# Kernel tuning notes

Measured on AMD Instinct MI355X. Metric: run time of the kernel, lower is better.

Reference implementation:

```python
import jax, jax.numpy as jnp
import numpy as np
import random

EPS = 1e-16  # matches EKM eps default
B, M, N, R = 8, 8192, 512, 256


def setup_inputs() -> dict:
    key = jax.random.key(0)
    kx, = jax.random.split(key, 1)
    x = jax.random.normal(kx, (B, M, N), dtype=jnp.float32)
    # EKM init: random.seed(42); inds = random.sample(range(M), R)
    random.seed(42)
    inds = jnp.asarray(random.sample(range(M), R), dtype=jnp.int32)
    # EKMInit overrides ekm.alpha with nn.Parameter(torch.tensor([0.1]))
    alpha = jnp.asarray([0.1], dtype=jnp.float32)
    return {"x": x, "alpha": alpha, "inds": inds}


def _memberships(x, v, alpha):
    x2 = jnp.sum(x * x, axis=2, keepdims=True)           # (B, M, 1)
    xv = jnp.einsum('bmn,bnr->bmr', x, v)                # (B, M, R)
    v2 = jnp.sum(v * v, axis=1, keepdims=True)           # (B, 1, R)
    d = jax.nn.relu(x2 - 2.0 * xv + v2)
    return jax.nn.softmax(-d / alpha, axis=2)            # (B, M, R)


def reference(x, alpha, inds):
    # init: v0 = t(x[:, inds, :]) -> (B, N, R); u0 = memberships(x, v0)
    v0 = jnp.swapaxes(x[:, inds, :], 1, 2)               # (B, N, R)
    # solver step (num_iters=1): u_new = memberships(x, v0) (== u0),
    # v_new = centers(x, u_new)
    u = _memberships(x, v0, alpha)                       # (B, M, R)
    u_n = (u + EPS) / (jnp.sum(u, axis=1, keepdims=True) + EPS)
    v = jnp.einsum('bmn,bmr->bnr', x, u_n)               # (B, N, R)
    return (u, v)
```

## Files before the change

kernel.cpp:

```cpp
#include <hip/hip_runtime.h>
#include <math.h>

#define B 8
#define M 8192
#define N 512
#define R 256
#define EPSF 1e-16f

typedef __attribute__((ext_vector_type(8))) short short8;
typedef __attribute__((ext_vector_type(16))) float f32x16;

__device__ __forceinline__ unsigned short bf16_rtn(float f) {
    unsigned int u = __float_as_uint(f);
    u += 0x7FFFu + ((u >> 16) & 1u);
    return (unsigned short)(u >> 16);
}

__device__ __forceinline__ void gll16(const unsigned short* g, unsigned short* l) {
    __builtin_amdgcn_global_load_lds(
        (const __attribute__((address_space(1))) unsigned int*)g,
        (__attribute__((address_space(3))) unsigned int*)l, 16, 0, 0);
}

__global__ __launch_bounds__(256) void ekm_kc(
    const float* __restrict__ x, const int* __restrict__ inds,
    unsigned short* __restrict__ c_hi, unsigned short* __restrict__ c_lo,
    float* __restrict__ v2g)
{
    const int t = threadIdx.x, b = blockIdx.y;
    const int r = blockIdx.x * 16 + (t >> 4);
    const int seg = (t & 15) * 32;
    const float* src = x + ((size_t)b * M + inds[r]) * N + seg;
    unsigned short* hd = c_hi + ((size_t)b * R + r) * 512 + seg;
    unsigned short* ld = c_lo + ((size_t)b * R + r) * 512 + seg;
    float vp = 0.f;
#pragma unroll
    for (int c = 0; c < 4; ++c) {
        float4 f0 = *(const float4*)(src + c * 8);
        float4 f1 = *(const float4*)(src + c * 8 + 4);
        float av[8] = {f0.x, f0.y, f0.z, f0.w, f1.x, f1.y, f1.z, f1.w};
        unsigned ph[4], pl[4];
#pragma unroll
        for (int j = 0; j < 4; ++j) {
            vp += av[2*j] * av[2*j] + av[2*j+1] * av[2*j+1];
            unsigned short h0 = bf16_rtn(av[2*j]), h1 = bf16_rtn(av[2*j+1]);
            float r0 = av[2*j]   - __uint_as_float((unsigned)h0 << 16);
            float r1 = av[2*j+1] - __uint_as_float((unsigned)h1 << 16);
            ph[j] = (unsigned)h0 | ((unsigned)h1 << 16);
            pl[j] = (unsigned)bf16_rtn(r0) | ((unsigned)bf16_rtn(r1) << 16);
        }
        *(uint4*)(hd + c * 8) = make_uint4(ph[0], ph[1], ph[2], ph[3]);
        *(uint4*)(ld + c * 8) = make_uint4(pl[0], pl[1], pl[2], pl[3]);
    }
    vp += __shfl_xor(vp, 1); vp += __shfl_xor(vp, 2);
    vp += __shfl_xor(vp, 4); vp += __shfl_xor(vp, 8);
    if ((t & 15) == 0) v2g[b * R + r] = vp;
}

__global__ __launch_bounds__(256, 4) void ekm_k1(
    const float* __restrict__ x, const float* __restrict__ alpha_p,
    const unsigned short* __restrict__ c_hi, const unsigned short* __restrict__ c_lo,
    const float* __restrict__ v2g, float* __restrict__ u_out,
    unsigned short* __restrict__ uT, unsigned short* __restrict__ xT,
    float* __restrict__ colsum)
{
    __shared__ unsigned short Ah[64 * 32], Al[64 * 32];
    __shared__ unsigned short Bh[256 * 32], Bl[256 * 32];

    const int t = threadIdx.x;
    const int b = blockIdx.y;
    const int m0 = blockIdx.x * 64;
    const int w = t >> 6, l = t & 63, col = l & 31, h5 = l >> 5;
    const int arow = t >> 2, kch = t & 3;
    const int cswz = (t & 3) ^ ((t >> 3) & 3);
    const int pswz = (col >> 1) & 3;
    const int aswz = (col >> 3) & 3;
    const int awi = arow * 32 + (kch ^ ((arow >> 3) & 3)) * 8;

    const float* ax = x + ((size_t)b * M + m0 + arow) * N + kch * 8;
    const unsigned short* bhs = c_hi + ((size_t)b * R + (t >> 2)) * 512 + cswz * 8;
    const unsigned short* bls = c_lo + ((size_t)b * R + (t >> 2)) * 512 + cswz * 8;

    f32x16 acc[2][2];
    acc[0][0] = (f32x16)0.f; acc[0][1] = (f32x16)0.f;
    acc[1][0] = (f32x16)0.f; acc[1][1] = (f32x16)0.f;

    float x2p = 0.f;
    float4 a0 = *(const float4*)(ax);
    float4 a1 = *(const float4*)(ax + 4);

    for (int k0 = 0; k0 < N; k0 += 32) {
        x2p += a0.x*a0.x + a0.y*a0.y + a0.z*a0.z + a0.w*a0.w
             + a1.x*a1.x + a1.y*a1.y + a1.z*a1.z + a1.w*a1.w;
        float av[8] = {a0.x, a0.y, a0.z, a0.w, a1.x, a1.y, a1.z, a1.w};
        unsigned ph[4], pl[4];
#pragma unroll
        for (int j = 0; j < 4; ++j) {
            unsigned short h0 = bf16_rtn(av[2*j]), h1 = bf16_rtn(av[2*j+1]);
            float r0 = av[2*j]   - __uint_as_float((unsigned)h0 << 16);
            float r1 = av[2*j+1] - __uint_as_float((unsigned)h1 << 16);
            ph[j] = (unsigned)h0 | ((unsigned)h1 << 16);
            pl[j] = (unsigned)bf16_rtn(r0) | ((unsigned)bf16_rtn(r1) << 16);
        }
        __syncthreads();
#pragma unroll
        for (int i = 0; i < 4; ++i) {
            gll16(bhs + k0 + i * (64 * 512), Bh + i * 2048 + t * 8);
            gll16(bls + k0 + i * (64 * 512), Bl + i * 2048 + t * 8);
        }
        *(uint4*)&Ah[awi] = make_uint4(ph[0], ph[1], ph[2], ph[3]);
        *(uint4*)&Al[awi] = make_uint4(pl[0], pl[1], pl[2], pl[3]);
        __syncthreads();

        if (k0 + 32 < N) {
            a0 = *(const float4*)(ax + k0 + 32);
            a1 = *(const float4*)(ax + k0 + 36);
        }

        {
            int kk = t >> 3, ms = (t & 7) * 8;
            unsigned short vv[8];
#pragma unroll
            for (int i = 0; i < 8; ++i) {
                int row = ms + i;
                vv[i] = Ah[row * 32 + (((kk >> 3) ^ ((row >> 3) & 3)) << 3) + (kk & 7)];
            }
            *(uint4*)(xT + ((size_t)b * N + k0 + kk) * M + m0 + ms) =
                make_uint4((unsigned)vv[0] | ((unsigned)vv[1] << 16),
                           (unsigned)vv[2] | ((unsigned)vv[3] << 16),
                           (unsigned)vv[4] | ((unsigned)vv[5] << 16),
                           (unsigned)vv[6] | ((unsigned)vv[7] << 16));
        }

#pragma unroll
        for (int half = 0; half < 2; ++half) {
            const int pa = (half * 2 + h5) ^ aswz;
            const int pc = (half * 2 + h5) ^ pswz;
            short8 ah[2], al2[2], bh[2], bl2[2];
#pragma unroll
            for (int tm = 0; tm < 2; ++tm) {
                ah[tm]  = *(const short8*)&Ah[(tm*32 + col) * 32 + pa * 8];
                al2[tm] = *(const short8*)&Al[(tm*32 + col) * 32 + pa * 8];
            }
#pragma unroll
            for (int tr = 0; tr < 2; ++tr) {
                bh[tr]  = *(const short8*)&Bh[(w*64 + tr*32 + col) * 32 + pc * 8];
                bl2[tr] = *(const short8*)&Bl[(w*64 + tr*32 + col) * 32 + pc * 8];
            }
#pragma unroll
            for (int tm = 0; tm < 2; ++tm)
#pragma unroll
            for (int tr = 0; tr < 2; ++tr) {
                acc[tm][tr] = __builtin_amdgcn_mfma_f32_32x32x16_bf16(ah[tm],  bh[tr],  acc[tm][tr], 0, 0, 0);
                acc[tm][tr] = __builtin_amdgcn_mfma_f32_32x32x16_bf16(ah[tm],  bl2[tr], acc[tm][tr], 0, 0, 0);
                acc[tm][tr] = __builtin_amdgcn_mfma_f32_32x32x16_bf16(al2[tm], bh[tr],  acc[tm][tr], 0, 0, 0);
            }
        }
    }

    __syncthreads();
    float* x2s = (float*)&Ah[0];
    float (*redm)[64] = (float (*)[64])&Al[0];
    float (*reds)[64] = (float (*)[64])&Bh[0];

    x2p += __shfl_xor(x2p, 1);
    x2p += __shfl_xor(x2p, 2);
    if (kch == 0) x2s[arow] = x2p;
    __syncthreads();

    const float ia = 1.4426950408889634f / alpha_p[0];
    float v2c[2];
#pragma unroll
    for (int tr = 0; tr < 2; ++tr)
        v2c[tr] = v2g[b * R + w * 64 + tr * 32 + col];

#pragma unroll
    for (int tm = 0; tm < 2; ++tm)
#pragma unroll
    for (int reg = 0; reg < 16; ++reg) {
        int rowl = (reg & 3) + 8 * (reg >> 2) + 4 * h5;
        float x2v = x2s[tm * 32 + rowl];
        float mn;
#pragma unroll
        for (int tr = 0; tr < 2; ++tr) {
            float d = x2v - 2.f * acc[tm][tr][reg] + v2c[tr];
            d = fmaxf(d, 0.f);
            acc[tm][tr][reg] = d;
            mn = (tr == 0) ? d : fminf(mn, d);
        }
        mn = fminf(mn, __shfl_xor(mn, 1));
        mn = fminf(mn, __shfl_xor(mn, 2));
        mn = fminf(mn, __shfl_xor(mn, 4));
        mn = fminf(mn, __shfl_xor(mn, 8));
        mn = fminf(mn, __shfl_xor(mn, 16));
        if (col == 0) redm[w][tm * 32 + rowl] = mn;
    }
    __syncthreads();

#pragma unroll
    for (int tm = 0; tm < 2; ++tm)
#pragma unroll
    for (int reg = 0; reg < 16; ++reg) {
        int m = tm * 32 + (reg & 3) + 8 * (reg >> 2) + 4 * h5;
        float mn = fminf(fminf(redm[0][m], redm[1][m]), fminf(redm[2][m], redm[3][m]));
        float s = 0.f;
#pragma unroll
        for (int tr = 0; tr < 2; ++tr) {
            float e = exp2f((mn - acc[tm][tr][reg]) * ia);
            acc[tm][tr][reg] = e;
            s += e;
        }
        s += __shfl_xor(s, 1); s += __shfl_xor(s, 2); s += __shfl_xor(s, 4);
        s += __shfl_xor(s, 8); s += __shfl_xor(s, 16);
        if (col == 0) reds[w][m] = s;
    }
    __syncthreads();

    float* ub = u_out + ((size_t)b * M + m0) * R + w * 64;
    float cs[2] = {0.f, 0.f};
#pragma unroll
    for (int tm = 0; tm < 2; ++tm)
#pragma unroll
    for (int reg = 0; reg < 16; ++reg) {
        int rowl = (reg & 3) + 8 * (reg >> 2) + 4 * h5;
        int m = tm * 32 + rowl;
        float inv = 1.f / (reds[0][m] + reds[1][m] + reds[2][m] + reds[3][m]);
#pragma unroll
        for (int tr = 0; tr < 2; ++tr) {
            float uu = acc[tm][tr][reg] * inv;
            acc[tm][tr][reg] = uu;
            ub[(size_t)m * R + tr * 32 + col] = uu;
            cs[tr] += uu;
        }
    }
    unsigned short* uTb = uT + ((size_t)b * R + w * 64) * M + m0;
#pragma unroll
    for (int tm = 0; tm < 2; ++tm)
#pragma unroll
    for (int tr = 0; tr < 2; ++tr)
#pragma unroll
    for (int rq = 0; rq < 4; ++rq) {
        uint2 p;
        p.x = (unsigned)bf16_rtn(acc[tm][tr][rq*4+0]) | ((unsigned)bf16_rtn(acc[tm][tr][rq*4+1]) << 16);
        p.y = (unsigned)bf16_rtn(acc[tm][tr][rq*4+2]) | ((unsigned)bf16_rtn(acc[tm][tr][rq*4+3]) << 16);
        *(uint2*)(uTb + (size_t)(tr*32 + col) * M + tm*32 + 8*rq + 4*h5) = p;
    }
    cs[0] += __shfl_xor(cs[0], 32);
    cs[1] += __shfl_xor(cs[1], 32);
    if (h5 == 0) {
        atomicAdd(&colsum[b * R + w * 64 + col], cs[0]);
        atomicAdd(&colsum[b * R + w * 64 + 32 + col], cs[1]);
    }
}

__global__ __launch_bounds__(256, 2) void ekm_k2(
    const unsigned short* __restrict__ xT, const unsigned short* __restrict__ uT,
    float* __restrict__ part)
{
    __shared__ unsigned short XA[128 * 32], UB[128 * 32];
    const int t = threadIdx.x;
    const int nt = blockIdx.x >> 1, rt = blockIdx.x & 1;
    const int slab = blockIdx.y, b = blockIdx.z;
    const int n0 = nt * 128, r0 = rt * 128;
    const int w = t >> 6, l = t & 63, col = l & 31, h5 = l >> 5;
    const int wn = w >> 1, wr = w & 1;
    const int cswz = (t & 3) ^ ((t >> 3) & 3);
    const int pswz = (col >> 1) & 3;

    const unsigned short* xs = xT + ((size_t)b * N + n0 + (t >> 2)) * M + slab * 1024 + cswz * 8;
    const unsigned short* us = uT + ((size_t)b * R + r0 + (t >> 2)) * M + slab * 1024 + cswz * 8;

    f32x16 acc[2][2];
    acc[0][0] = (f32x16)0.f; acc[0][1] = (f32x16)0.f;
    acc[1][0] = (f32x16)0.f; acc[1][1] = (f32x16)0.f;

    for (int k0 = 0; k0 < 1024; k0 += 32) {
        __syncthreads();
#pragma unroll
        for (int i = 0; i < 2; ++i) {
            gll16(xs + k0 + (size_t)i * 64 * M, XA + i * 2048 + t * 8);
            gll16(us + k0 + (size_t)i * 64 * M, UB + i * 2048 + t * 8);
        }
        __syncthreads();
#pragma unroll
        for (int half = 0; half < 2; ++half) {
            const int pc = (half * 2 + h5) ^ pswz;
            short8 af[2], bf2[2];
#pragma unroll
            for (int tm = 0; tm < 2; ++tm)
                af[tm] = *(const short8*)&XA[(wn*64 + tm*32 + col) * 32 + pc*8];
#pragma unroll
            for (int tr = 0; tr < 2; ++tr)
                bf2[tr] = *(const short8*)&UB[(wr*64 + tr*32 + col) * 32 + pc*8];
#pragma unroll
            for (int tm = 0; tm < 2; ++tm)
#pragma unroll
            for (int tr = 0; tr < 2; ++tr)
                acc[tm][tr] = __builtin_amdgcn_mfma_f32_32x32x16_bf16(af[tm], bf2[tr], acc[tm][tr], 0, 0, 0);
        }
    }

    float* pb = part + (size_t)slab * ((size_t)B * N * R) + (size_t)b * N * R;
#pragma unroll
    for (int tm = 0; tm < 2; ++tm)
#pragma unroll
    for (int reg = 0; reg < 16; ++reg) {
        int n = n0 + wn*64 + tm*32 + (reg & 3) + 8*(reg >> 2) + 4*h5;
#pragma unroll
        for (int tr = 0; tr < 2; ++tr)
            pb[(size_t)n * R + r0 + wr*64 + tr*32 + col] = acc[tm][tr][reg];
    }
}

__global__ __launch_bounds__(256) void ekm_red(
    const float* __restrict__ part, const float* __restrict__ colsum,
    float* __restrict__ v_out)
{
    size_t o = ((size_t)blockIdx.x * 256 + threadIdx.x) * 4;
    float sx = 0.f, sy = 0.f, sz = 0.f, sw = 0.f;
#pragma unroll
    for (int sl = 0; sl < 8; ++sl) {
        float4 p = *(const float4*)(part + (size_t)sl * B * N * R + o);
        sx += p.x; sy += p.y; sz += p.z; sw += p.w;
    }
    int b = (int)(o >> 17);
    int r = (int)(o & (R - 1));
    float4 cs = *(const float4*)(colsum + b * R + r);
    float4 vo;
    vo.x = sx / (cs.x + EPSF);
    vo.y = sy / (cs.y + EPSF);
    vo.z = sz / (cs.z + EPSF);
    vo.w = sw / (cs.w + EPSF);
    *(float4*)(v_out + o) = vo;
}

extern "C" void kernel_launch(void* const* d_in, const int* in_sizes, int n_in,
                              void* d_out, int out_size, void* d_ws, size_t ws_size,
                              hipStream_t stream) {
    const float* x     = (const float*)d_in[0];
    const float* alpha = (const float*)d_in[1];
    const int*   inds  = (const int*)d_in[2];

    float* u_out = (float*)d_out;
    float* v_out = u_out + (size_t)B * M * R;

    char* ws = (char*)d_ws;
    const size_t CH = (size_t)B * R * 512 * 2;
    unsigned short* c_hi   = (unsigned short*)ws;
    unsigned short* c_lo   = (unsigned short*)(ws + CH);
    float*          v2g    = (float*)(ws + 2 * CH);
    float*          colsum = (float*)(ws + 2 * CH + (size_t)B * R * 4);
    char* p = ws + 2 * CH + 2 * (size_t)B * R * 4;
    unsigned short* xT = (unsigned short*)p;          p += (size_t)B * N * M * 2;
    unsigned short* uT = (unsigned short*)p;          p += (size_t)B * R * M * 2;
    float*          part = (float*)p;

    hipMemsetAsync(colsum, 0, (size_t)B * R * sizeof(float), stream);

    ekm_kc<<<dim3(16, B), 256, 0, stream>>>(x, inds, c_hi, c_lo, v2g);
    ekm_k1<<<dim3(M / 64, B), 256, 0, stream>>>(x, alpha, c_hi, c_lo, v2g,
                                                u_out, uT, xT, colsum);
    ekm_k2<<<dim3(8, 8, B), 256, 0, stream>>>(xT, uT, part);
    ekm_red<<<(B * N * R / 4) / 256, 256, 0, stream>>>(part, colsum, v_out);
}
```

Measured before the change: 341.8 us.

## Halve k1 row tile and software-pipeline global loads through registers

The first GEMM kernel now processes 32 rows of x per block instead of 64, doubling the grid. The B operand (centers) is loaded into registers one k-step ahead rather than via direct global-to-LDS loads, and the A conversion is overlapped with the MFMA work using explicit barriers and sched_barriers. The aim is to hide global memory latency and raise parallelism. In exchange, each block reuses the B tile over half as many rows, so the centers are read from global memory twice as often, and register pressure rises.

```diff
diff --git a/kernel.cpp b/kernel.cpp
--- a/kernel.cpp
+++ b/kernel.cpp
@@ -64,108 +64,137 @@
     unsigned short* __restrict__ uT, unsigned short* __restrict__ xT,
     float* __restrict__ colsum)
 {
-    __shared__ unsigned short Ah[64 * 32], Al[64 * 32];
+    __shared__ unsigned short Ah[32 * 32], Al[32 * 32];
     __shared__ unsigned short Bh[256 * 32], Bl[256 * 32];
 
     const int t = threadIdx.x;
     const int b = blockIdx.y;
-    const int m0 = blockIdx.x * 64;
+    const int m0 = blockIdx.x * 32;
     const int w = t >> 6, l = t & 63, col = l & 31, h5 = l >> 5;
-    const int arow = t >> 2, kch = t & 3;
+    const int arow = t >> 3, kc8 = t & 7;
     const int cswz = (t & 3) ^ ((t >> 3) & 3);
     const int pswz = (col >> 1) & 3;
     const int aswz = (col >> 3) & 3;
-    const int awi = arow * 32 + (kch ^ ((arow >> 3) & 3)) * 8;
-
-    const float* ax = x + ((size_t)b * M + m0 + arow) * N + kch * 8;
+    const int awi = arow * 32 + ((kc8 >> 1) ^ ((arow >> 3) & 3)) * 8 + (kc8 & 1) * 4;
+
+    const float* ax = x + ((size_t)b * M + m0 + arow) * N + kc8 * 4;
     const unsigned short* bhs = c_hi + ((size_t)b * R + (t >> 2)) * 512 + cswz * 8;
     const unsigned short* bls = c_lo + ((size_t)b * R + (t >> 2)) * 512 + cswz * 8;
 
-    f32x16 acc[2][2];
-    acc[0][0] = (f32x16)0.f; acc[0][1] = (f32x16)0.f;
-    acc[1][0] = (f32x16)0.f; acc[1][1] = (f32x16)0.f;
+    f32x16 acc[2];
+    acc[0] = (f32x16)0.f; acc[1] = (f32x16)0.f;
 
     float x2p = 0.f;
-    float4 a0 = *(const float4*)(ax);
-    float4 a1 = *(const float4*)(ax + 4);
-
-    for (int k0 = 0; k0 < N; k0 += 32) {
-        x2p += a0.x*a0.x + a0.y*a0.y + a0.z*a0.z + a0.w*a0.w
-             + a1.x*a1.x + a1.y*a1.y + a1.z*a1.z + a1.w*a1.w;
-        float av[8] = {a0.x, a0.y, a0.z, a0.w, a1.x, a1.y, a1.z, a1.w};
-        unsigned ph[4], pl[4];
-#pragma unroll
-        for (int j = 0; j < 4; ++j) {
-            unsigned short h0 = bf16_rtn(av[2*j]), h1 = bf16_rtn(av[2*j+1]);
-            float r0 = av[2*j]   - __uint_as_float((unsigned)h0 << 16);
-            float r1 = av[2*j+1] - __uint_as_float((unsigned)h1 << 16);
-            ph[j] = (unsigned)h0 | ((unsigned)h1 << 16);
-            pl[j] = (unsigned)bf16_rtn(r0) | ((unsigned)bf16_rtn(r1) << 16);
-        }
-        __syncthreads();
+    float4 a0;
+    unsigned ph0, ph1, pl0, pl1;
+    uint4 rbh[4], rbl[4];
+
+    auto loadB = [&](int k0) {
 #pragma unroll
         for (int i = 0; i < 4; ++i) {
-            gll16(bhs + k0 + i * (64 * 512), Bh + i * 2048 + t * 8);
-            gll16(bls + k0 + i * (64 * 512), Bl + i * 2048 + t * 8);
-        }
-        *(uint4*)&Ah[awi] = make_uint4(ph[0], ph[1], ph[2], ph[3]);
-        *(uint4*)&Al[awi] = make_uint4(pl[0], pl[1], pl[2], pl[3]);
-        __syncthreads();
-
-        if (k0 + 32 < N) {
-            a0 = *(const float4*)(ax + k0 + 32);
-            a1 = *(const float4*)(ax + k0 + 36);
-        }
-
-        {
-            int kk = t >> 3, ms = (t & 7) * 8;
-            unsigned short vv[8];
-#pragma unroll
-            for (int i = 0; i < 8; ++i) {
-                int row = ms + i;
-                vv[i] = Ah[row * 32 + (((kk >> 3) ^ ((row >> 3) & 3)) << 3) + (kk & 7)];
-            }
-            *(uint4*)(xT + ((size_t)b * N + k0 + kk) * M + m0 + ms) =
-                make_uint4((unsigned)vv[0] | ((unsigned)vv[1] << 16),
-                           (unsigned)vv[2] | ((unsigned)vv[3] << 16),
-                           (unsigned)vv[4] | ((unsigned)vv[5] << 16),
-                           (unsigned)vv[6] | ((unsigned)vv[7] << 16));
-        }
-
+            rbh[i] = *(const uint4*)(bhs + k0 + i * (64 * 512));
+            rbl[i] = *(const uint4*)(bls + k0 + i * (64 * 512));
+        }
+    };
+    auto writeB = [&](void) {
+#pragma unroll
+        for (int i = 0; i < 4; ++i) {
+            *(uint4*)&Bh[i * 2048 + t * 8] = rbh[i];
+            *(uint4*)&Bl[i * 2048 + t * 8] = rbl[i];
+        }
+    };
+    auto convertA = [&](void) {
+        float av[4] = {a0.x, a0.y, a0.z, a0.w};
+        x2p += av[0]*av[0] + av[1]*av[1] + av[2]*av[2] + av[3]*av[3];
+        unsigned short h0 = bf16_rtn(av[0]), h1 = bf16_rtn(av[1]);
+        unsigned short h2 = bf16_rtn(av[2]), h3 = bf16_rtn(av[3]);
+        float r0 = av[0] - __uint_as_float((unsigned)h0 << 16);
+        float r1 = av[1] - __uint_as_float((unsigned)h1 << 16);
+        float r2 = av[2] - __uint_as_float((unsigned)h2 << 16);
+        float r3 = av[3] - __uint_as_float((unsigned)h3 << 16);
+        ph0 = (unsigned)h0 | ((unsigned)h1 << 16);
+        ph1 = (unsigned)h2 | ((unsigned)h3 << 16);
+        pl0 = (unsigned)bf16_rtn(r0) | ((unsigned)bf16_rtn(r1) << 16);
+        pl1 = (unsigned)bf16_rtn(r2) | ((unsigned)bf16_rtn(r3) << 16);
+    };
+    auto writeA = [&](void) {
+        *(uint2*)&Ah[awi] = make_uint2(ph0, ph1);
+        *(uint2*)&Al[awi] = make_uint2(pl0, pl1);
+    };
+    auto mfma_tile = [&](void) {
 #pragma unroll
         for (int half = 0; half < 2; ++half) {
             const int pa = (half * 2 + h5) ^ aswz;
             const int pc = (half * 2 + h5) ^ pswz;
-            short8 ah[2], al2[2], bh[2], bl2[2];
-#pragma unroll
-            for (int tm = 0; tm < 2; ++tm) {
-                ah[tm]  = *(const short8*)&Ah[(tm*32 + col) * 32 + pa * 8];
-                al2[tm] = *(const short8*)&Al[(tm*32 + col) * 32 + pa * 8];
-            }
+            short8 ah = *(const short8*)&Ah[col * 32 + pa * 8];
+            short8 al = *(const short8*)&Al[col * 32 + pa * 8];
+            short8 bh[2], bl2[2];
 #pragma unroll
             for (int tr = 0; tr < 2; ++tr) {
                 bh[tr]  = *(const short8*)&Bh[(w*64 + tr*32 + col) * 32 + pc * 8];
                 bl2[tr] = *(const short8*)&Bl[(w*64 + tr*32 + col) * 32 + pc * 8];
             }
 #pragma unroll
-            for (int tm = 0; tm < 2; ++tm)
-#pragma unroll
             for (int tr = 0; tr < 2; ++tr) {
-                acc[tm][tr] = __builtin_amdgcn_mfma_f32_32x32x16_bf16(ah[tm],  bh[tr],  acc[tm][tr], 0, 0, 0);
-                acc[tm][tr] = __builtin_amdgcn_mfma_f32_32x32x16_bf16(ah[tm],  bl2[tr], acc[tm][tr], 0, 0, 0);
-                acc[tm][tr] = __builtin_amdgcn_mfma_f32_32x32x16_bf16(al2[tm], bh[tr],  acc[tm][tr], 0, 0, 0);
+                acc[tr] = __builtin_amdgcn_mfma_f32_32x32x16_bf16(ah, bh[tr],  acc[tr], 0, 0, 0);
+                acc[tr] = __builtin_amdgcn_mfma_f32_32x32x16_bf16(ah, bl2[tr], acc[tr], 0, 0, 0);
+                acc[tr] = __builtin_amdgcn_mfma_f32_32x32x16_bf16(al, bh[tr],  acc[tr], 0, 0, 0);
             }
         }
-    }
+    };
+    auto xt_store = [&](int k0) {
+        int kk = t >> 3, ms = (t & 7) * 4;
+        unsigned short vv[4];
+#pragma unroll
+        for (int j = 0; j < 4; ++j) {
+            int row = ms + j;
+            vv[j] = Ah[row * 32 + (((kk >> 3) ^ ((row >> 3) & 3)) << 3) + (kk & 7)];
+        }
+        *(uint2*)(xT + ((size_t)b * N + k0 + kk) * M + m0 + ms) =
+            make_uint2((unsigned)vv[0] | ((unsigned)vv[1] << 16),
+                       (unsigned)vv[2] | ((unsigned)vv[3] << 16));
+    };
+
+    a0 = *(const float4*)(ax);
+    loadB(0);
+    convertA();
+    writeA(); writeB();
+    a0 = *(const float4*)(ax + 32);
+    loadB(32);
+    asm volatile("s_waitcnt lgkmcnt(0)" ::: "memory");
+    __builtin_amdgcn_sched_barrier(0);
+    __builtin_amdgcn_s_barrier();
+    __builtin_amdgcn_sched_barrier(0);
+
+    for (int k0 = 0; k0 < N - 32; k0 += 32) {
+        xt_store(k0);
+        mfma_tile();
+        convertA();
+        __builtin_amdgcn_sched_barrier(0);
+        __builtin_amdgcn_s_barrier();
+        __builtin_amdgcn_sched_barrier(0);
+        writeA(); writeB();
+        if (k0 + 64 < N) {
+            a0 = *(const float4*)(ax + k0 + 64);
+            loadB(k0 + 64);
+        }
+        asm volatile("s_waitcnt lgkmcnt(0)" ::: "memory");
+        __builtin_amdgcn_sched_barrier(0);
+        __builtin_amdgcn_s_barrier();
+        __builtin_amdgcn_sched_barrier(0);
+    }
+    xt_store(N - 32);
+    mfma_tile();
 
     __syncthreads();
     float* x2s = (float*)&Ah[0];
-    float (*redm)[64] = (float (*)[64])&Al[0];
-    float (*reds)[64] = (float (*)[64])&Bh[0];
+    float (*redm)[32] = (float (*)[32])&Al[0];
+    float (*reds)[32] = (float (*)[32])&Bh[0];
 
     x2p += __shfl_xor(x2p, 1);
     x2p += __shfl_xor(x2p, 2);
-    if (kch == 0) x2s[arow] = x2p;
+    x2p += __shfl_xor(x2p, 4);
+    if (kc8 == 0) x2s[arow] = x2p;
     __syncthreads();
 
     const float ia = 1.4426950408889634f / alpha_p[0];
@@ -175,17 +204,15 @@
         v2c[tr] = v2g[b * R + w * 64 + tr * 32 + col];
 
 #pragma unroll
-    for (int tm = 0; tm < 2; ++tm)
-#pragma unroll
     for (int reg = 0; reg < 16; ++reg) {
         int rowl = (reg & 3) + 8 * (reg >> 2) + 4 * h5;
-        float x2v = x2s[tm * 32 + rowl];
+        float x2v = x2s[rowl];
         float mn;
 #pragma unroll
         for (int tr = 0; tr < 2; ++tr) {
-            float d = x2v - 2.f * acc[tm][tr][reg] + v2c[tr];
+            float d = x2v - 2.f * acc[tr][reg] + v2c[tr];
             d = fmaxf(d, 0.f);
-            acc[tm][tr][reg] = d;
+            acc[tr][reg] = d;
             mn = (tr == 0) ? d : fminf(mn, d);
         }
         mn = fminf(mn, __shfl_xor(mn, 1));
@@ -193,21 +220,19 @@
         mn = fminf(mn, __shfl_xor(mn, 4));
         mn = fminf(mn, __shfl_xor(mn, 8));
         mn = fminf(mn, __shfl_xor(mn, 16));
-        if (col == 0) redm[w][tm * 32 + rowl] = mn;
+        if (col == 0) redm[w][rowl] = mn;
     }
     __syncthreads();
 
 #pragma unroll
-    for (int tm = 0; tm < 2; ++tm)
-#pragma unroll
     for (int reg = 0; reg < 16; ++reg) {
-        int m = tm * 32 + (reg & 3) + 8 * (reg >> 2) + 4 * h5;
+        int m = (reg & 3) + 8 * (reg >> 2) + 4 * h5;
         float mn = fminf(fminf(redm[0][m], redm[1][m]), fminf(redm[2][m], redm[3][m]));
         float s = 0.f;
 #pragma unroll
         for (int tr = 0; tr < 2; ++tr) {
-            float e = exp2f((mn - acc[tm][tr][reg]) * ia);
-            acc[tm][tr][reg] = e;
+            float e = exp2f((mn - acc[tr][reg]) * ia);
+            acc[tr][reg] = e;
             s += e;
         }
         s += __shfl_xor(s, 1); s += __shfl_xor(s, 2); s += __shfl_xor(s, 4);
@@ -219,31 +244,26 @@
     float* ub = u_out + ((size_t)b * M + m0) * R + w * 64;
     float cs[2] = {0.f, 0.f};
 #pragma unroll
-    for (int tm = 0; tm < 2; ++tm)
-#pragma unroll
     for (int reg = 0; reg < 16; ++reg) {
-        int rowl = (reg & 3) + 8 * (reg >> 2) + 4 * h5;
-        int m = tm * 32 + rowl;
+        int m = (reg & 3) + 8 * (reg >> 2) + 4 * h5;
         float inv = 1.f / (reds[0][m] + reds[1][m] + reds[2][m] + reds[3][m]);
 #pragma unroll
         for (int tr = 0; tr < 2; ++tr) {
-            float uu = acc[tm][tr][reg] * inv;
-            acc[tm][tr][reg] = uu;
+            float uu = acc[tr][reg] * inv;
+            acc[tr][reg] = uu;
             ub[(size_t)m * R + tr * 32 + col] = uu;
             cs[tr] += uu;
         }
     }
     unsigned short* uTb = uT + ((size_t)b * R + w * 64) * M + m0;
 #pragma unroll
-    for (int tm = 0; tm < 2; ++tm)
-#pragma unroll
     for (int tr = 0; tr < 2; ++tr)
 #pragma unroll
     for (int rq = 0; rq < 4; ++rq) {
         uint2 p;
-        p.x = (unsigned)bf16_rtn(acc[tm][tr][rq*4+0]) | ((unsigned)bf16_rtn(acc[tm][tr][rq*4+1]) << 16);
-        p.y = (unsigned)bf16_rtn(acc[tm][tr][rq*4+2]) | ((unsigned)bf16_rtn(acc[tm][tr][rq*4+3]) << 16);
-        *(uint2*)(uTb + (size_t)(tr*32 + col) * M + tm*32 + 8*rq + 4*h5) = p;
+        p.x = (unsigned)bf16_rtn(acc[tr][rq*4+0]) | ((unsigned)bf16_rtn(acc[tr][rq*4+1]) << 16);
+        p.y = (unsigned)bf16_rtn(acc[tr][rq*4+2]) | ((unsigned)bf16_rtn(acc[tr][rq*4+3]) << 16);
+        *(uint2*)(uTb + (size_t)(tr*32 + col) * M + 8*rq + 4*h5) = p;
     }
     cs[0] += __shfl_xor(cs[0], 32);
     cs[1] += __shfl_xor(cs[1], 32);
@@ -358,7 +378,7 @@
     hipMemsetAsync(colsum, 0, (size_t)B * R * sizeof(float), stream);
 
     ekm_kc<<<dim3(16, B), 256, 0, stream>>>(x, inds, c_hi, c_lo, v2g);
-    ekm_k1<<<dim3(M / 64, B), 256, 0, stream>>>(x, alpha, c_hi, c_lo, v2g,
+    ekm_k1<<<dim3(M / 32, B), 256, 0, stream>>>(x, alpha, c_hi, c_lo, v2g,
                                                 u_out, uT, xT, colsum);
     ekm_k2<<<dim3(8, 8, B), 256, 0, stream>>>(xT, uT, part);
     ekm_red<<<(B * N * R / 4) / 256, 256, 0, stream>>>(part, colsum, v_out);
```

Result: slower. 690.2 us (+101.9%).

## Load centers directly into registers in MFMA-fragment layout with double buffering

Applied to the files above, without the earlier changes.

The center matrix (hi/lo bf16 split) is now written by the prep kernel in a layout that matches the MFMA operand fragments. The main kernel loads B fragments straight from global memory into registers, double-buffered across k-steps, instead of staging them through LDS with global_load_lds. This removes the large B tiles from shared memory, along with their LDS traffic and part of the barrier work. Blocks are also reordered so batch varies fastest, and the occupancy hint drops from 4 to 3 to leave room for the extra fragment registers. The risks are redundant global and L2 reads of B by each block, and reduced occupancy.

```diff
diff --git a/kernel.cpp b/kernel.cpp
--- a/kernel.cpp
+++ b/kernel.cpp
@@ -24,15 +24,16 @@
 
 __global__ __launch_bounds__(256) void ekm_kc(
     const float* __restrict__ x, const int* __restrict__ inds,
-    unsigned short* __restrict__ c_hi, unsigned short* __restrict__ c_lo,
+    unsigned short* __restrict__ cpH, unsigned short* __restrict__ cpL,
     float* __restrict__ v2g)
 {
     const int t = threadIdx.x, b = blockIdx.y;
     const int r = blockIdx.x * 16 + (t >> 4);
     const int seg = (t & 15) * 32;
+    const int rg = r >> 5, rl = r & 31;
     const float* src = x + ((size_t)b * M + inds[r]) * N + seg;
-    unsigned short* hd = c_hi + ((size_t)b * R + r) * 512 + seg;
-    unsigned short* ld = c_lo + ((size_t)b * R + r) * 512 + seg;
+    unsigned short* hb = cpH + (((size_t)b * 32 + (seg >> 4)) * 8 + rg) * 512;
+    unsigned short* lb = cpL + (((size_t)b * 32 + (seg >> 4)) * 8 + rg) * 512;
     float vp = 0.f;
 #pragma unroll
     for (int c = 0; c < 4; ++c) {
@@ -49,119 +50,151 @@
             ph[j] = (unsigned)h0 | ((unsigned)h1 << 16);
             pl[j] = (unsigned)bf16_rtn(r0) | ((unsigned)bf16_rtn(r1) << 16);
         }
-        *(uint4*)(hd + c * 8) = make_uint4(ph[0], ph[1], ph[2], ph[3]);
-        *(uint4*)(ld + c * 8) = make_uint4(pl[0], pl[1], pl[2], pl[3]);
+        const size_t off = (size_t)(c >> 1) * 4096 + (size_t)((c & 1) * 32 + rl) * 8;
+        *(uint4*)(hb + off) = make_uint4(ph[0], ph[1], ph[2], ph[3]);
+        *(uint4*)(lb + off) = make_uint4(pl[0], pl[1], pl[2], pl[3]);
     }
     vp += __shfl_xor(vp, 1); vp += __shfl_xor(vp, 2);
     vp += __shfl_xor(vp, 4); vp += __shfl_xor(vp, 8);
     if ((t & 15) == 0) v2g[b * R + r] = vp;
 }
 
-__global__ __launch_bounds__(256, 4) void ekm_k1(
+__global__ __launch_bounds__(256, 3) void ekm_k1(
     const float* __restrict__ x, const float* __restrict__ alpha_p,
-    const unsigned short* __restrict__ c_hi, const unsigned short* __restrict__ c_lo,
+    const unsigned short* __restrict__ cpH, const unsigned short* __restrict__ cpL,
     const float* __restrict__ v2g, float* __restrict__ u_out,
     unsigned short* __restrict__ uT, unsigned short* __restrict__ xT,
     float* __restrict__ colsum)
 {
     __shared__ unsigned short Ah[64 * 32], Al[64 * 32];
-    __shared__ unsigned short Bh[256 * 32], Bl[256 * 32];
 
     const int t = threadIdx.x;
-    const int b = blockIdx.y;
-    const int m0 = blockIdx.x * 64;
+    const int bid = blockIdx.x;
+    const int b = bid & 7;
+    const int m0 = (bid >> 3) * 64;
     const int w = t >> 6, l = t & 63, col = l & 31, h5 = l >> 5;
     const int arow = t >> 2, kch = t & 3;
-    const int cswz = (t & 3) ^ ((t >> 3) & 3);
-    const int pswz = (col >> 1) & 3;
     const int aswz = (col >> 3) & 3;
     const int awi = arow * 32 + (kch ^ ((arow >> 3) & 3)) * 8;
 
     const float* ax = x + ((size_t)b * M + m0 + arow) * N + kch * 8;
-    const unsigned short* bhs = c_hi + ((size_t)b * R + (t >> 2)) * 512 + cswz * 8;
-    const unsigned short* bls = c_lo + ((size_t)b * R + (t >> 2)) * 512 + cswz * 8;
+    const unsigned short* bpH = cpH + (((size_t)b * 256 + w * 2) * 64 + l) * 8;
+    const unsigned short* bpL = cpL + (((size_t)b * 256 + w * 2) * 64 + l) * 8;
 
     f32x16 acc[2][2];
     acc[0][0] = (f32x16)0.f; acc[0][1] = (f32x16)0.f;
     acc[1][0] = (f32x16)0.f; acc[1][1] = (f32x16)0.f;
 
     float x2p = 0.f;
-    float4 a0 = *(const float4*)(ax);
-    float4 a1 = *(const float4*)(ax + 4);
-
-    for (int k0 = 0; k0 < N; k0 += 32) {
-        x2p += a0.x*a0.x + a0.y*a0.y + a0.z*a0.z + a0.w*a0.w
-             + a1.x*a1.x + a1.y*a1.y + a1.z*a1.z + a1.w*a1.w;
+    float4 a0, a1;
+    unsigned ph[4], pl[4];
+    short8 cbh[2][2], cbl[2][2], nbh[2][2], nbl[2][2];
+
+    auto loadB = [&](int kc0, short8 (&bh)[2][2], short8 (&bl)[2][2]) {
+#pragma unroll
+        for (int half = 0; half < 2; ++half)
+#pragma unroll
+        for (int tr = 0; tr < 2; ++tr) {
+            const size_t o = (size_t)(kc0 + half) * 4096 + (size_t)tr * 512;
+            bh[half][tr] = *(const short8*)(bpH + o);
+            bl[half][tr] = *(const short8*)(bpL + o);
+        }
+    };
+    auto convertA = [&](void) {
         float av[8] = {a0.x, a0.y, a0.z, a0.w, a1.x, a1.y, a1.z, a1.w};
-        unsigned ph[4], pl[4];
 #pragma unroll
         for (int j = 0; j < 4; ++j) {
+            x2p += av[2*j] * av[2*j] + av[2*j+1] * av[2*j+1];
             unsigned short h0 = bf16_rtn(av[2*j]), h1 = bf16_rtn(av[2*j+1]);
             float r0 = av[2*j]   - __uint_as_float((unsigned)h0 << 16);
             float r1 = av[2*j+1] - __uint_as_float((unsigned)h1 << 16);
             ph[j] = (unsigned)h0 | ((unsigned)h1 << 16);
             pl[j] = (unsigned)bf16_rtn(r0) | ((unsigned)bf16_rtn(r1) << 16);
         }
-        __syncthreads();
-#pragma unroll
-        for (int i = 0; i < 4; ++i) {
-            gll16(bhs + k0 + i * (64 * 512), Bh + i * 2048 + t * 8);
-            gll16(bls + k0 + i * (64 * 512), Bl + i * 2048 + t * 8);
-        }
+    };
+    auto writeA = [&](void) {
         *(uint4*)&Ah[awi] = make_uint4(ph[0], ph[1], ph[2], ph[3]);
         *(uint4*)&Al[awi] = make_uint4(pl[0], pl[1], pl[2], pl[3]);
-        __syncthreads();
-
-        if (k0 + 32 < N) {
-            a0 = *(const float4*)(ax + k0 + 32);
-            a1 = *(const float4*)(ax + k0 + 36);
-        }
-
-        {
-            int kk = t >> 3, ms = (t & 7) * 8;
-            unsigned short vv[8];
-#pragma unroll
-            for (int i = 0; i < 8; ++i) {
-                int row = ms + i;
-                vv[i] = Ah[row * 32 + (((kk >> 3) ^ ((row >> 3) & 3)) << 3) + (kk & 7)];
-            }
-            *(uint4*)(xT + ((size_t)b * N + k0 + kk) * M + m0 + ms) =
-                make_uint4((unsigned)vv[0] | ((unsigned)vv[1] << 16),
-                           (unsigned)vv[2] | ((unsigned)vv[3] << 16),
-                           (unsigned)vv[4] | ((unsigned)vv[5] << 16),
-                           (unsigned)vv[6] | ((unsigned)vv[7] << 16));
-        }
-
+    };
+    auto mfma_tile = [&](short8 (&bh)[2][2], short8 (&bl)[2][2]) {
 #pragma unroll
         for (int half = 0; half < 2; ++half) {
             const int pa = (half * 2 + h5) ^ aswz;
-            const int pc = (half * 2 + h5) ^ pswz;
-            short8 ah[2], al2[2], bh[2], bl2[2];
+            short8 ah[2], al2[2];
 #pragma unroll
             for (int tm = 0; tm < 2; ++tm) {
                 ah[tm]  = *(const short8*)&Ah[(tm*32 + col) * 32 + pa * 8];
                 al2[tm] = *(const short8*)&Al[(tm*32 + col) * 32 + pa * 8];
             }
 #pragma unroll
+            for (int tm = 0; tm < 2; ++tm)
+#pragma unroll
             for (int tr = 0; tr < 2; ++tr) {
-                bh[tr]  = *(const short8*)&Bh[(w*64 + tr*32 + col) * 32 + pc * 8];
-                bl2[tr] = *(const short8*)&Bl[(w*64 + tr*32 + col) * 32 + pc * 8];
+                acc[tm][tr] = __builtin_amdgcn_mfma_f32_32x32x16_bf16(ah[tm],  bh[half][tr], acc[tm][tr], 0, 0, 0);
+                acc[tm][tr] = __builtin_amdgcn_mfma_f32_32x32x16_bf16(ah[tm],  bl[half][tr], acc[tm][tr], 0, 0, 0);
+                acc[tm][tr] = __builtin_amdgcn_mfma_f32_32x32x16_bf16(al2[tm], bh[half][tr], acc[tm][tr], 0, 0, 0);
             }
-#pragma unroll
-            for (int tm = 0; tm < 2; ++tm)
-#pragma unroll
-            for (int tr = 0; tr < 2; ++tr) {
-                acc[tm][tr] = __builtin_amdgcn_mfma_f32_32x32x16_bf16(ah[tm],  bh[tr],  acc[tm][tr], 0, 0, 0);
-                acc[tm][tr] = __builtin_amdgcn_mfma_f32_32x32x16_bf16(ah[tm],  bl2[tr], acc[tm][tr], 0, 0, 0);
-                acc[tm][tr] = __builtin_amdgcn_mfma_f32_32x32x16_bf16(al2[tm], bh[tr],  acc[tm][tr], 0, 0, 0);
+        }
+    };
+    auto xt_store = [&](int k0) {
+        int kk = t >> 3, ms = (t & 7) * 8;
+        unsigned short vv[8];
+#pragma unroll
+        for (int i = 0; i < 8; ++i) {
+            int row = ms + i;
+            vv[i] = Ah[row * 32 + (((kk >> 3) ^ ((row >> 3) & 3)) << 3) + (kk & 7)];
+        }
+        *(uint4*)(xT + ((size_t)b * N + k0 + kk) * M + m0 + ms) =
+            make_uint4((unsigned)vv[0] | ((unsigned)vv[1] << 16),
+                       (unsigned)vv[2] | ((unsigned)vv[3] << 16),
+                       (unsigned)vv[4] | ((unsigned)vv[5] << 16),
+                       (unsigned)vv[6] | ((unsigned)vv[7] << 16));
+    };
+
+    a0 = *(const float4*)(ax);
+    a1 = *(const float4*)(ax + 4);
+    loadB(0, cbh, cbl);
+    convertA();
+    writeA();
+    a0 = *(const float4*)(ax + 32);
+    a1 = *(const float4*)(ax + 36);
+    loadB(2, nbh, nbl);
+    asm volatile("s_waitcnt lgkmcnt(0)" ::: "memory");
+    __builtin_amdgcn_sched_barrier(0);
+    __builtin_amdgcn_s_barrier();
+    __builtin_amdgcn_sched_barrier(0);
+
+    auto step = [&](int kk, short8 (&ch)[2][2], short8 (&cl)[2][2]) {
+        xt_store(kk);
+        mfma_tile(ch, cl);
+        if (kk + 64 < N) loadB((kk + 64) >> 4, ch, cl);
+        if (kk + 32 < N) {
+            convertA();
+            __builtin_amdgcn_sched_barrier(0);
+            __builtin_amdgcn_s_barrier();
+            __builtin_amdgcn_sched_barrier(0);
+            writeA();
+            if (kk + 64 < N) {
+                a0 = *(const float4*)(ax + kk + 64);
+                a1 = *(const float4*)(ax + kk + 68);
             }
-        }
+            asm volatile("s_waitcnt lgkmcnt(0)" ::: "memory");
+            __builtin_amdgcn_sched_barrier(0);
+            __builtin_amdgcn_s_barrier();
+            __builtin_amdgcn_sched_barrier(0);
+        }
+    };
+
+#pragma unroll 1
+    for (int k0 = 0; k0 < N; k0 += 64) {
+        step(k0, cbh, cbl);
+        step(k0 + 32, nbh, nbl);
     }
 
     __syncthreads();
     float* x2s = (float*)&Ah[0];
     float (*redm)[64] = (float (*)[64])&Al[0];
-    float (*reds)[64] = (float (*)[64])&Bh[0];
+    float (*reds)[64] = (float (*)[64])((float*)&Al[0] + 256);
 
     x2p += __shfl_xor(x2p, 1);
     x2p += __shfl_xor(x2p, 2);
@@ -346,8 +379,8 @@
 
     char* ws = (char*)d_ws;
     const size_t CH = (size_t)B * R * 512 * 2;
-    unsigned short* c_hi   = (unsigned short*)ws;
-    unsigned short* c_lo   = (unsigned short*)(ws + CH);
+    unsigned short* cpH    = (unsigned short*)ws;
+    unsigned short* cpL    = (unsigned short*)(ws + CH);
     float*          v2g    = (float*)(ws + 2 * CH);
     float*          colsum = (float*)(ws + 2 * CH + (size_t)B * R * 4);
     char* p = ws + 2 * CH + 2 * (size_t)B * R * 4;
@@ -357,9 +390,9 @@
 
     hipMemsetAsync(colsum, 0, (size_t)B * R * sizeof(float), stream);
 
-    ekm_kc<<<dim3(16, B), 256, 0, stream>>>(x, inds, c_hi, c_lo, v2g);
-    ekm_k1<<<dim3(M / 64, B), 256, 0, stream>>>(x, alpha, c_hi, c_lo, v2g,
-                                                u_out, uT, xT, colsum);
+    ekm_kc<<<dim3(16, B), 256, 0, stream>>>(x, inds, cpH, cpL, v2g);
+    ekm_k1<<<dim3(M / 64 * B), 256, 0, stream>>>(x, alpha, cpH, cpL, v2g,
+                                                 u_out, uT, xT, colsum);
     ekm_k2<<<dim3(8, 8, B), 256, 0, stream>>>(xT, uT, part);
     ekm_red<<<(B * N * R / 4) / 256, 256, 0, stream>>>(part, colsum, v_out);
 }
```

New measurement: 409.7 us. 19.9% more time.
